# Performance work log

Measured on AMD Instinct MI355X. Metric: run time of the kernel, lower is better.

## Reference

```python
import jax, jax.numpy as jnp
import numpy as np

N, E, B = 16384, 65536, 32
D_IN, ED, H, L = 4, 5, 64, 3  # node feat, edge feat, hidden=output, num layers
NEG_SLOPE = 0.1
EPS = 1e-5


def _leaky(v):
    return jnp.where(v > 0, v, NEG_SLOPE * v)


def setup_inputs() -> dict:
    key = jax.random.key(0)
    ks = jax.random.split(key, 32)
    s = 0.05
    inp = {
        'x': jax.random.normal(ks[0], (N, D_IN), jnp.float32),
        'edge_index': jax.random.randint(ks[1], (2, E), 0, N),
        'edge_attr': jax.random.normal(ks[2], (E, ED), jnp.float32),
        'batch': jnp.sort(jax.random.randint(ks[3], (N,), 0, B)),
        # input projection Linear(4 -> H)
        'W_in': s * jax.random.normal(ks[4], (H, D_IN), jnp.float32),
        'b_in': jnp.zeros((H,), jnp.float32),
        # per-layer edge MLP: Linear(ED->H), Linear(H->H), Linear(H->H*H); stacked over L
        'ew1': s * jax.random.normal(ks[5], (L, H, ED), jnp.float32),
        'eb1': jnp.zeros((L, H), jnp.float32),
        'ew2': s * jax.random.normal(ks[6], (L, H, H), jnp.float32),
        'eb2': jnp.zeros((L, H), jnp.float32),
        'ew3': s * jax.random.normal(ks[7], (L, H * H, H), jnp.float32),
        'eb3': jnp.zeros((L, H * H), jnp.float32),
        # NNConv root weight + bias per layer
        'root_w': s * jax.random.normal(ks[8], (L, H, H), jnp.float32),
        'root_b': jnp.zeros((L, H), jnp.float32),
        # LayerNorm per layer
        'ln_g': jnp.ones((L, H), jnp.float32),
        'ln_b': jnp.zeros((L, H), jnp.float32),
        # prediction head: Linear(H->H), Linear(H->H//2), Linear(H//2->1)
        'pw1': s * jax.random.normal(ks[9], (H, H), jnp.float32),
        'pb1': jnp.zeros((H,), jnp.float32),
        'pw2': s * jax.random.normal(ks[10], (H // 2, H), jnp.float32),
        'pb2': jnp.zeros((H // 2,), jnp.float32),
        'pw3': s * jax.random.normal(ks[11], (1, H // 2), jnp.float32),
        'pb3': jnp.zeros((1,), jnp.float32),
    }
    return inp


def reference(x, edge_index, edge_attr, batch, W_in, b_in, ew1, eb1, ew2, eb2,
              ew3, eb3, root_w, root_b, ln_g, ln_b, pw1, pb1, pw2, pb2, pw3, pb3):
    src, dst = edge_index[0], edge_index[1]
    n_nodes = x.shape[0]
    n_edges = edge_attr.shape[0]
    # in-degree for scatter-mean (PyG yields 0 for isolated nodes)
    deg = jax.ops.segment_sum(jnp.ones((n_edges,), x.dtype), dst, num_segments=n_nodes)
    deg = jnp.maximum(deg, 1.0)[:, None]

    # input projection (dropout = identity in eval)
    h = _leaky(x @ W_in.T + b_in)

    for l in range(L):
        # edge MLP -> per-edge weight matrix [E, H, H]
        e = _leaky(edge_attr @ ew1[l].T + eb1[l])
        e = _leaky(e @ ew2[l].T + eb2[l])
        Wf = (e @ ew3[l].T + eb3[l]).reshape(n_edges, H, H)
        # message = x_src @ W_edge, scatter-mean to dst
        msg = jnp.einsum('ei,eio->eo', h[src], Wf)
        agg = jax.ops.segment_sum(msg, dst, num_segments=n_nodes) / deg
        out = agg + h @ root_w[l].T + root_b[l]
        # LayerNorm (post-norm)
        mu = out.mean(-1, keepdims=True)
        var = ((out - mu) ** 2).mean(-1, keepdims=True)
        out = (out - mu) * jax.lax.rsqrt(var + EPS) * ln_g[l] + ln_b[l]
        # activation + (identity) dropout + residual (in==out for all layers)
        h = _leaky(out) + h

    # global mean pool over graphs
    pooled = jax.ops.segment_sum(h, batch, num_segments=B)
    cnt = jax.ops.segment_sum(jnp.ones((n_nodes,), h.dtype), batch, num_segments=B)
    pooled = pooled / jnp.maximum(cnt, 1.0)[:, None]

    # prediction head
    p = _leaky(pooled @ pw1.T + pb1)
    p = _leaky(p @ pw2.T + pb2)
    pred = (p @ pw3.T + pb3).squeeze(-1)  # [B]
    return pred
```

## Files before the change

kernel.cpp:

```cpp
#include <hip/hip_runtime.h>
#include <hip/hip_bf16.h>

#define N_NODES 16384
#define N_EDGES 65536
#define NB      32
#define H       64
#define NLAYERS 3
#define NEG     0.1f
#define LN_EPS  1e-5f

typedef _Float16 f16;
typedef _Float16 f16x2 __attribute__((ext_vector_type(2)));
typedef _Float16 f16x8 __attribute__((ext_vector_type(8)));
typedef __fp16   hf16x2 __attribute__((ext_vector_type(2)));
typedef float    f32x16 __attribute__((ext_vector_type(16)));

union F16x8 { f16x8 v; f16x2 p[4]; int4 i4; int2 i2[2]; };
union F16x2U { f16x2 h2; hf16x2 raw; unsigned int u; };
union F16U   { f16 h; unsigned short u; };

__device__ __forceinline__ f16x2 pkrtz(float a, float b) {
    F16x2U t; t.raw = __builtin_amdgcn_cvt_pkrtz(a, b); return t.h2;
}
__device__ __forceinline__ float leaky(float v) { return v > 0.f ? v : NEG * v; }

__global__ __launch_bounds__(256) void k_setup(const float* __restrict__ x,
                                               const float* __restrict__ Win,
                                               const float* __restrict__ bin,
                                               const int* __restrict__ dst,
                                               const float* __restrict__ ew3,
                                               const float* __restrict__ eb3,
                                               float* __restrict__ h,
                                               float* __restrict__ deg,
                                               f16* __restrict__ Bp) {
    int bid = blockIdx.x;
    if (bid < 4096) {
        int t = bid * 256 + threadIdx.x;
        int n = t >> 6, j = t & 63;
        const float* xr = x + n * 4;
        const float* wr = Win + j * 4;
        float v = bin[j] + xr[0] * wr[0] + xr[1] * wr[1] + xr[2] * wr[2] + xr[3] * wr[3];
        h[t] = leaky(v);
    } else if (bid < 4352) {
        int e = (bid - 4096) * 256 + threadIdx.x;
        atomicAdd(&deg[dst[e]], 1.0f);
    } else {
        int tg    = (bid - 4352) * 256 + threadIdx.x;
        int lane  = tg & 63;
        int gslot = tg >> 6;
        int l     = gslot / 520;
        int slot  = gslot - l * 520;
        const float* ew3l = ew3 + (size_t)l * 262144;
        const float* eb3l = eb3 + (size_t)l * 4096;
        int i   = slot >> 3;
        int rem = slot & 7;
        int ks  = rem >> 1;
        int oq  = rem & 1;
        int o   = oq * 32 + (lane & 31);
        int k0  = ks * 16 + (lane >> 5) * 8;
        float v[8];
        if (i < 64) {
            const float* s = ew3l + ((size_t)(i * 64 + o)) * 64 + k0;
            float4 a = ((const float4*)s)[0];
            float4 b = ((const float4*)s)[1];
            v[0] = a.x; v[1] = a.y; v[2] = a.z; v[3] = a.w;
            v[4] = b.x; v[5] = b.y; v[6] = b.z; v[7] = b.w;
        } else {
#pragma unroll
            for (int j = 0; j < 8; j++) v[j] = eb3l[(k0 + j) * 64 + o];
        }
        union { int4 i4; f16 a[8]; } out;
#pragma unroll
        for (int j = 0; j < 8; j++) out.a[j] = (f16)v[j];
        *(int4*)(Bp + (size_t)l * 266240 + (size_t)slot * 512 + lane * 8) = out.i4;
    }
}

#define HS_STRIDE 76

__device__ __forceinline__ void loadB8(const f16* __restrict__ Bp, int c, int oq, int lane, F16x8* dstB) {
    const f16* base = Bp + (((size_t)(c * 16 + oq)) << 9) + lane * 8;
#pragma unroll
    for (int di = 0; di < 2; di++)
#pragma unroll
        for (int ks = 0; ks < 4; ks++)
            dstB[di * 4 + ks].i4 = *(const int4*)(base + ((di * 8 + ks * 2) << 9));
}
__device__ __forceinline__ void loadB4(const f16* __restrict__ Bp, int oq, int lane, F16x8* dstB) {
    const f16* base = Bp + (((size_t)(512 + oq)) << 9) + lane * 8;
#pragma unroll
    for (int ks = 0; ks < 4; ks++)
        dstB[ks].i4 = *(const int4*)(base + ((ks * 2) << 9));
}

__device__ __forceinline__ void msg_chunk2(int c, const F16x8* __restrict__ B,
                                           const unsigned short* hp0,
                                           const unsigned short* hp1,
                                           const f16x2 (*e2p)[4][4], f32x16* CC) {
    unsigned int rr0 = *(const unsigned int*)(hp0 + 2 * c);
    unsigned int rr1 = *(const unsigned int*)(hp1 + 2 * c);
    F16x2U h00, h01, h10, h11;
    h00.u = __builtin_amdgcn_perm(rr0, rr0, 0x01000100u);
    h10.u = __builtin_amdgcn_perm(rr0, rr0, 0x03020302u);
    h01.u = __builtin_amdgcn_perm(rr1, rr1, 0x01000100u);
    h11.u = __builtin_amdgcn_perm(rr1, rr1, 0x03020302u);
#pragma unroll
    for (int ks = 0; ks < 4; ks++) {
        F16x8 A00, A01, A10, A11;
#pragma unroll
        for (int r = 0; r < 4; r++) {
            A00.p[r] = h00.h2 * e2p[0][ks][r];
            A01.p[r] = h01.h2 * e2p[1][ks][r];
            A10.p[r] = h10.h2 * e2p[0][ks][r];
            A11.p[r] = h11.h2 * e2p[1][ks][r];
        }
        CC[0] = __builtin_amdgcn_mfma_f32_32x32x16_f16(A00.v, B[0 * 4 + ks].v, CC[0], 0, 0, 0);
        CC[1] = __builtin_amdgcn_mfma_f32_32x32x16_f16(A01.v, B[0 * 4 + ks].v, CC[1], 0, 0, 0);
        CC[2] = __builtin_amdgcn_mfma_f32_32x32x16_f16(A10.v, B[1 * 4 + ks].v, CC[2], 0, 0, 0);
        CC[3] = __builtin_amdgcn_mfma_f32_32x32x16_f16(A11.v, B[1 * 4 + ks].v, CC[3], 0, 0, 0);
    }
}

__global__ __launch_bounds__(256, 2) void k_msg(const float* __restrict__ h,
                                                const float* __restrict__ ea,
                                                const float* __restrict__ w1,
                                                const float* __restrict__ b1,
                                                const float* __restrict__ w2,
                                                const float* __restrict__ b2,
                                                const f16* __restrict__ Bp,
                                                const int* __restrict__ src,
                                                const int* __restrict__ dst,
                                                float* __restrict__ agg) {
    __shared__ __align__(16) unsigned short hsL[128 * HS_STRIDE];
    __shared__ __align__(16) unsigned short e1L[128 * 72];
    __shared__ __align__(16) unsigned short e2L[128 * 72];
    __shared__ float eas[128 * 8];
    __shared__ int dstL[128];

    const int t    = threadIdx.x;
    const int lane = t & 63;
    const int w    = t >> 6;
    const int eh   = w >> 1, oq = w & 1;
    const int m    = lane & 31;
    const int kp   = lane >> 5;
    const int eb   = blockIdx.x * 128;

    for (int idx = t; idx < 640; idx += 256) {
        int r = idx / 5, d = idx - r * 5;
        eas[r * 8 + d] = ea[(size_t)eb * 5 + idx];
    }
    {
        int e    = t >> 1;
        int half = t & 1;
        int nsrc = src[eb + e];
        const float4* hr = (const float4*)(h + (size_t)nsrc * 64 + half * 32);
        unsigned int* hrow = (unsigned int*)hsL + e * (HS_STRIDE / 2) + half * 16;
#pragma unroll
        for (int q = 0; q < 8; q++) {
            float4 v = hr[q];
            F16x2U p0, p1;
            p0.raw = __builtin_amdgcn_cvt_pkrtz(v.x, v.y);
            p1.raw = __builtin_amdgcn_cvt_pkrtz(v.z, v.w);
            hrow[q * 2 + 0] = p0.u;
            hrow[q * 2 + 1] = p1.u;
        }
        if (t < 128) dstL[t] = dst[eb + t];
    }
    __syncthreads();

    {
        int kk = t & 63;
        int eg = t >> 6;
        float w1r[5];
#pragma unroll
        for (int d = 0; d < 5; d++) w1r[d] = w1[kk * 5 + d];
        float b1r = b1[kk];
#pragma unroll 4
        for (int g = 0; g < 32; g++) {
            int row = eg * 32 + g;
            float4 a4 = *(const float4*)(eas + row * 8);
            float a5 = eas[row * 8 + 4];
            float v = b1r + a4.x * w1r[0] + a4.y * w1r[1] + a4.z * w1r[2] + a4.w * w1r[3] + a5 * w1r[4];
            F16U z; z.h = (f16)leaky(v);
            e1L[row * 72 + kk] = z.u;
        }
    }
    __syncthreads();

    {
        F16x8 W2f[4];
#pragma unroll
        for (int ks = 0; ks < 4; ks++) {
            const float* s = w2 + (size_t)(oq * 32 + m) * 64 + ks * 16 + kp * 8;
            float4 a = ((const float4*)s)[0];
            float4 b = ((const float4*)s)[1];
            W2f[ks].p[0] = pkrtz(a.x, a.y);
            W2f[ks].p[1] = pkrtz(a.z, a.w);
            W2f[ks].p[2] = pkrtz(b.x, b.y);
            W2f[ks].p[3] = pkrtz(b.z, b.w);
        }
        float b2r = b2[oq * 32 + m];
#pragma unroll
        for (int tt = 0; tt < 2; tt++) {
            f32x16 C2 = {0,0,0,0,0,0,0,0,0,0,0,0,0,0,0,0};
#pragma unroll
            for (int ks = 0; ks < 4; ks++) {
                F16x8 A;
                A.i4 = *(const int4*)(e1L + (size_t)((eh * 2 + tt) * 32 + m) * 72 + ks * 16 + kp * 8);
                C2 = __builtin_amdgcn_mfma_f32_32x32x16_f16(A.v, W2f[ks].v, C2, 0, 0, 0);
            }
#pragma unroll
            for (int reg = 0; reg < 16; reg++) {
                int r = (reg & 3) + 8 * (reg >> 2) + 4 * kp;
                F16U z; z.h = (f16)leaky(C2[reg] + b2r);
                e2L[((eh * 2 + tt) * 32 + r) * 72 + oq * 32 + m] = z.u;
            }
        }
    }
    __syncthreads();

    f16x2 e2p[2][4][4];
#pragma unroll
    for (int tt = 0; tt < 2; tt++) {
#pragma unroll
        for (int ks = 0; ks < 4; ks++) {
            F16x8 q;
            q.i4 = *(const int4*)(e2L + (size_t)((eh * 2 + tt) * 32 + m) * 72 + ks * 16 + kp * 8);
            e2p[tt][ks][0] = q.p[0]; e2p[tt][ks][1] = q.p[1];
            e2p[tt][ks][2] = q.p[2]; e2p[tt][ks][3] = q.p[3];
        }
    }

    f32x16 CC[4];
#pragma unroll
    for (int q = 0; q < 4; q++)
#pragma unroll
        for (int r = 0; r < 16; r++) CC[q][r] = 0.f;

    const unsigned short* hp0 = hsL + ((eh * 2 + 0) * 32 + m) * HS_STRIDE;
    const unsigned short* hp1 = hsL + ((eh * 2 + 1) * 32 + m) * HS_STRIDE;

    F16x8 B0[8], B1[8];
    loadB8(Bp, 0, oq, lane, B0);
    loadB8(Bp, 1, oq, lane, B1);
    for (int it = 0; it < 15; it++) {
        int c = it * 2;
        msg_chunk2(c,     B0, hp0, hp1, e2p, CC);  loadB8(Bp, c + 2, oq, lane, B0);
        msg_chunk2(c + 1, B1, hp0, hp1, e2p, CC);  loadB8(Bp, c + 3, oq, lane, B1);
    }
    msg_chunk2(30, B0, hp0, hp1, e2p, CC);
    loadB4(Bp, oq, lane, B0);
    msg_chunk2(31, B1, hp0, hp1, e2p, CC);

#pragma unroll
    for (int ks = 0; ks < 4; ks++) {
        int koff = (ks * 16 + kp * 8) * 2;
        const char* r0p = (const char*)hsL + (size_t)((eh * 2 + 0) * 32 + m) * (HS_STRIDE * 2) + koff;
        const char* r1p = (const char*)hsL + (size_t)((eh * 2 + 1) * 32 + m) * (HS_STRIDE * 2) + koff;
        F16x8 A0, A1;
        A0.i2[0] = *(const int2*)(r0p); A0.i2[1] = *(const int2*)(r0p + 8);
        A1.i2[0] = *(const int2*)(r1p); A1.i2[1] = *(const int2*)(r1p + 8);
        CC[0] = __builtin_amdgcn_mfma_f32_32x32x16_f16(A0.v, B0[ks].v, CC[0], 0, 0, 0);
        CC[1] = __builtin_amdgcn_mfma_f32_32x32x16_f16(A1.v, B0[ks].v, CC[1], 0, 0, 0);
    }

    int o = oq * 32 + m;
#pragma unroll
    for (int reg = 0; reg < 16; reg++) {
        int r = (reg & 3) + 8 * (reg >> 2) + 4 * kp;
        atomicAdd(&agg[(size_t)dstL[(eh * 2 + 0) * 32 + r] * 64 + o], CC[0][reg] + CC[2][reg]);
    }
#pragma unroll
    for (int reg = 0; reg < 16; reg++) {
        int r = (reg & 3) + 8 * (reg >> 2) + 4 * kp;
        atomicAdd(&agg[(size_t)dstL[(eh * 2 + 1) * 32 + r] * 64 + o], CC[1][reg] + CC[3][reg]);
    }
}

__global__ __launch_bounds__(512) void k_node(const float* __restrict__ agg,
                                              const float* __restrict__ deg,
                                              const float* __restrict__ rw,
                                              const float* __restrict__ rb,
                                              const float* __restrict__ lg,
                                              const float* __restrict__ lb,
                                              float* __restrict__ h,
                                              const int* __restrict__ batch,
                                              float* __restrict__ pooled,
                                              int last) {
    __shared__ __align__(16) unsigned short hA[64 * 72];
    __shared__ float outL[64][68];
    int t = threadIdx.x;
    int nb = blockIdx.x * 64;
    int lane = t & 63, w = t >> 6;
    int m = lane & 31, kp = lane >> 5;

    int node = t >> 3, c0 = (t & 7) * 8;
    size_t gb = (size_t)(nb + node) * 64 + c0;
    float4 ag0 = *(const float4*)(agg + gb);
    float4 ag1 = *(const float4*)(agg + gb + 4);
    float4 hp0 = *(const float4*)(h + gb);
    float4 hp1 = *(const float4*)(h + gb + 4);
    float  vdeg = fmaxf(deg[nb + node], 1.0f);
    float4 gv0 = *(const float4*)(lg + c0);
    float4 gv1 = *(const float4*)(lg + c0 + 4);
    float4 bv0 = *(const float4*)(lb + c0);
    float4 bv1 = *(const float4*)(lb + c0 + 4);

    {
        unsigned int* drow = (unsigned int*)hA + node * 36 + c0 / 2;
        F16x2U p0, p1, p2, p3;
        p0.raw = __builtin_amdgcn_cvt_pkrtz(hp0.x, hp0.y);
        p1.raw = __builtin_amdgcn_cvt_pkrtz(hp0.z, hp0.w);
        p2.raw = __builtin_amdgcn_cvt_pkrtz(hp1.x, hp1.y);
        p3.raw = __builtin_amdgcn_cvt_pkrtz(hp1.z, hp1.w);
        drow[0] = p0.u; drow[1] = p1.u; drow[2] = p2.u; drow[3] = p3.u;
    }
    F16x8 Bf[4];
    if (t < 256) {
        int oq = w & 1;
#pragma unroll
        for (int ks = 0; ks < 4; ks++) {
            const float* s = rw + (size_t)(oq * 32 + m) * 64 + ks * 16 + kp * 8;
            float4 a = ((const float4*)s)[0];
            float4 b = ((const float4*)s)[1];
            Bf[ks].p[0] = pkrtz(a.x, a.y);
            Bf[ks].p[1] = pkrtz(a.z, a.w);
            Bf[ks].p[2] = pkrtz(b.x, b.y);
            Bf[ks].p[3] = pkrtz(b.z, b.w);
        }
    }
    __syncthreads();

    if (t < 256) {
        int nq = w >> 1, oq = w & 1;
        f32x16 C = {0,0,0,0,0,0,0,0,0,0,0,0,0,0,0,0};
#pragma unroll
        for (int ks = 0; ks < 4; ks++) {
            F16x8 A;
            A.i4 = *(const int4*)(hA + (size_t)(nq * 32 + m) * 72 + ks * 16 + kp * 8);
            C = __builtin_amdgcn_mfma_f32_32x32x16_f16(A.v, Bf[ks].v, C, 0, 0, 0);
        }
        int o = oq * 32 + m;
        float rbv = rb[o];
#pragma unroll
        for (int reg = 0; reg < 16; reg++) {
            int r = (reg & 3) + 8 * (reg >> 2) + 4 * kp;
            outL[nq * 32 + r][o] = C[reg] + rbv;
        }
    }
    __syncthreads();

    {
        float v[8];
        v[0] = outL[node][c0 + 0] + ag0.x / vdeg;
        v[1] = outL[node][c0 + 1] + ag0.y / vdeg;
        v[2] = outL[node][c0 + 2] + ag0.z / vdeg;
        v[3] = outL[node][c0 + 3] + ag0.w / vdeg;
        v[4] = outL[node][c0 + 4] + ag1.x / vdeg;
        v[5] = outL[node][c0 + 5] + ag1.y / vdeg;
        v[6] = outL[node][c0 + 6] + ag1.z / vdeg;
        v[7] = outL[node][c0 + 7] + ag1.w / vdeg;
        float s = 0.f;
#pragma unroll
        for (int i = 0; i < 8; i++) s += v[i];
        s += __shfl_xor(s, 1);
        s += __shfl_xor(s, 2);
        s += __shfl_xor(s, 4);
        float mu = s * (1.f / 64.f);
        float vs = 0.f;
#pragma unroll
        for (int i = 0; i < 8; i++) { float d = v[i] - mu; vs += d * d; }
        vs += __shfl_xor(vs, 1);
        vs += __shfl_xor(vs, 2);
        vs += __shfl_xor(vs, 4);
        float rs = rsqrtf(vs * (1.f / 64.f) + LN_EPS);
        float gfv[8] = { gv0.x, gv0.y, gv0.z, gv0.w, gv1.x, gv1.y, gv1.z, gv1.w };
        float bfv[8] = { bv0.x, bv0.y, bv0.z, bv0.w, bv1.x, bv1.y, bv1.z, bv1.w };
        float hfv[8] = { hp0.x, hp0.y, hp0.z, hp0.w, hp1.x, hp1.y, hp1.z, hp1.w };
        float hn[8];
#pragma unroll
        for (int i = 0; i < 8; i++) {
            float ov = (v[i] - mu) * rs * gfv[i] + bfv[i];
            hn[i] = leaky(ov) + hfv[i];
        }
        float4 hw0, hw1;
        hw0.x = hn[0]; hw0.y = hn[1]; hw0.z = hn[2]; hw0.w = hn[3];
        hw1.x = hn[4]; hw1.y = hn[5]; hw1.z = hn[6]; hw1.w = hn[7];
        *(float4*)(h + gb)     = hw0;
        *(float4*)(h + gb + 4) = hw1;
#pragma unroll
        for (int i = 0; i < 8; i++) outL[node][c0 + i] = hn[i];
    }

    if (last) {
        __syncthreads();
        float accp = 0.f;
        int cur = batch[nb + w * 8];
        for (int q = 0; q < 8; q++) {
            int n = w * 8 + q;
            float hv = outL[n][lane];
            int b = batch[nb + n];
            if (b != cur) { atomicAdd(&pooled[cur * 64 + lane], accp); accp = 0.f; cur = b; }
            accp += hv;
        }
        atomicAdd(&pooled[cur * 64 + lane], accp);
    }
}

__global__ __launch_bounds__(256) void k_head(const float* __restrict__ pooled,
                                              const int* __restrict__ batch,
                                              const float* __restrict__ pw1, const float* __restrict__ pb1,
                                              const float* __restrict__ pw2, const float* __restrict__ pb2,
                                              const float* __restrict__ pw3, const float* __restrict__ pb3,
                                              float* __restrict__ out) {
    __shared__ float cntL[32];
    __shared__ float ps[32][64];
    __shared__ float p1[32][64];
    __shared__ float p2[32][32];
    int t = threadIdx.x;
    if (t < 32) cntL[t] = 0.f;
    __syncthreads();
    {
        const int4* bp4 = (const int4*)(batch + t * 64);
        int cur = batch[t * 64];
        float c = 0.f;
        for (int q = 0; q < 16; q++) {
            int4 b4 = bp4[q];
            int bs[4] = { b4.x, b4.y, b4.z, b4.w };
#pragma unroll
            for (int e = 0; e < 4; e++) {
                if (bs[e] != cur) { atomicAdd(&cntL[cur], c); cur = bs[e]; c = 0.f; }
                c += 1.f;
            }
        }
        atomicAdd(&cntL[cur], c);
    }
    __syncthreads();
    for (int idx = t; idx < 2048; idx += 256) {
        int b = idx >> 6, j = idx & 63;
        ps[b][j] = pooled[idx] / fmaxf(cntL[b], 1.0f);
    }
    __syncthreads();
    for (int idx = t; idx < 2048; idx += 256) {
        int b = idx >> 6, j = idx & 63;
        float v = pb1[j];
#pragma unroll 8
        for (int i = 0; i < 64; i++) v += ps[b][i] * pw1[j * 64 + i];
        p1[b][j] = leaky(v);
    }
    __syncthreads();
    for (int idx = t; idx < 1024; idx += 256) {
        int b = idx >> 5, j = idx & 31;
        float v = pb2[j];
#pragma unroll 8
        for (int i = 0; i < 64; i++) v += p1[b][i] * pw2[j * 64 + i];
        p2[b][j] = leaky(v);
    }
    __syncthreads();
    if (t < 32) {
        float v = pb3[0];
#pragma unroll 8
        for (int i = 0; i < 32; i++) v += p2[t][i] * pw3[i];
        out[t] = v;
    }
}

extern "C" void kernel_launch(void* const* d_in, const int* in_sizes, int n_in,
                              void* d_out, int out_size, void* d_ws, size_t ws_size,
                              hipStream_t stream) {
    const float* x    = (const float*)d_in[0];
    const int*   eidx = (const int*)  d_in[1];
    const float* ea   = (const float*)d_in[2];
    const int*   bat  = (const int*)  d_in[3];
    const float* Win  = (const float*)d_in[4];
    const float* bin  = (const float*)d_in[5];
    const float* ew1  = (const float*)d_in[6];
    const float* eb1  = (const float*)d_in[7];
    const float* ew2  = (const float*)d_in[8];
    const float* eb2  = (const float*)d_in[9];
    const float* ew3  = (const float*)d_in[10];
    const float* eb3  = (const float*)d_in[11];
    const float* rw   = (const float*)d_in[12];
    const float* rb   = (const float*)d_in[13];
    const float* lg   = (const float*)d_in[14];
    const float* lb   = (const float*)d_in[15];
    const float* pw1  = (const float*)d_in[16];
    const float* pb1  = (const float*)d_in[17];
    const float* pw2  = (const float*)d_in[18];
    const float* pb2  = (const float*)d_in[19];
    const float* pw3  = (const float*)d_in[20];
    const float* pb3  = (const float*)d_in[21];
    float* out = (float*)d_out;

    float* ws     = (float*)d_ws;
    float* h      = ws;
    float* agg    = ws + 1048576;
    float* deg    = ws + 4194304;
    float* pooled = ws + 4210688;
    f16*   Bp     = (f16*)(ws + 4212800);

    const int* srcp = eidx;
    const int* dstp = eidx + N_EDGES;

    (void)hipMemsetAsync(agg, 0, (size_t)3164224 * sizeof(float), stream);

    k_setup<<<4742, 256, 0, stream>>>(x, Win, bin, dstp, ew3, eb3, h, deg, Bp);

    for (int l = 0; l < NLAYERS; l++) {
        float* agg_l = agg + (size_t)l * N_NODES * H;
        k_msg <<<N_EDGES / 128, 256, 0, stream>>>(h, ea, ew1 + l * 320, eb1 + l * 64,
                                                  ew2 + l * 4096, eb2 + l * 64,
                                                  Bp + (size_t)l * 266240,
                                                  srcp, dstp, agg_l);
        k_node<<<N_NODES / 64, 512, 0, stream>>>(agg_l, deg, rw + l * 4096, rb + l * 64,
                                                 lg + l * 64, lb + l * 64, h,
                                                 bat, pooled, l == NLAYERS - 1 ? 1 : 0);
    }

    k_head<<<1, 256, 0, stream>>>(pooled, bat, pw1, pb1, pw2, pb2, pw3, pb3, out);
}
```

Baseline: 305.5 us.

## Fuse all GNN stages into one persistent cooperative kernel with grid syncs

Replaces the sequence of setup, per-layer message, per-layer node and head launches with a single cooperative kernel of 256 blocks × 512 threads. The phases are separated by grid-wide barriers, and shared memory is reused through a union. The message phase now handles 256 edges per block and stages the per-edge weight tiles into an LDS triple-buffer ring using global_load_lds, so loads overlap the MFMA work. The aim is to remove launch gaps and improve reuse of the B matrix. The costs are grid-sync overhead, lower occupancy from one large block per CU, and a fallback path to the old kernels if the cooperative launch fails.

```diff
diff --git a/kernel.cpp b/kernel.cpp
--- a/kernel.cpp
+++ b/kernel.cpp
@@ -1,5 +1,8 @@
 #include <hip/hip_runtime.h>
 #include <hip/hip_bf16.h>
+#include <hip/hip_cooperative_groups.h>
+
+namespace cg = cooperative_groups;
 
 #define N_NODES 16384
 #define N_EDGES 65536
@@ -23,6 +26,484 @@
     F16x2U t; t.raw = __builtin_amdgcn_cvt_pkrtz(a, b); return t.h2;
 }
 __device__ __forceinline__ float leaky(float v) { return v > 0.f ? v : NEG * v; }
+
+#define HS_STRIDE 76
+
+__device__ __forceinline__ void loadB8(const f16* __restrict__ Bp, int c, int oq, int lane, F16x8* dstB) {
+    const f16* base = Bp + (((size_t)(c * 16 + oq)) << 9) + lane * 8;
+#pragma unroll
+    for (int di = 0; di < 2; di++)
+#pragma unroll
+        for (int ks = 0; ks < 4; ks++)
+            dstB[di * 4 + ks].i4 = *(const int4*)(base + ((di * 8 + ks * 2) << 9));
+}
+__device__ __forceinline__ void loadB4(const f16* __restrict__ Bp, int oq, int lane, F16x8* dstB) {
+    const f16* base = Bp + (((size_t)(512 + oq)) << 9) + lane * 8;
+#pragma unroll
+    for (int ks = 0; ks < 4; ks++)
+        dstB[ks].i4 = *(const int4*)(base + ((ks * 2) << 9));
+}
+__device__ __forceinline__ void msg_chunk2(int c, const F16x8* __restrict__ B,
+                                           const unsigned short* hp0,
+                                           const unsigned short* hp1,
+                                           const f16x2 (*e2p)[4][4], f32x16* CC) {
+    unsigned int rr0 = *(const unsigned int*)(hp0 + 2 * c);
+    unsigned int rr1 = *(const unsigned int*)(hp1 + 2 * c);
+    F16x2U h00, h01, h10, h11;
+    h00.u = __builtin_amdgcn_perm(rr0, rr0, 0x01000100u);
+    h10.u = __builtin_amdgcn_perm(rr0, rr0, 0x03020302u);
+    h01.u = __builtin_amdgcn_perm(rr1, rr1, 0x01000100u);
+    h11.u = __builtin_amdgcn_perm(rr1, rr1, 0x03020302u);
+#pragma unroll
+    for (int ks = 0; ks < 4; ks++) {
+        F16x8 A00, A01, A10, A11;
+#pragma unroll
+        for (int r = 0; r < 4; r++) {
+            A00.p[r] = h00.h2 * e2p[0][ks][r];
+            A01.p[r] = h01.h2 * e2p[1][ks][r];
+            A10.p[r] = h10.h2 * e2p[0][ks][r];
+            A11.p[r] = h11.h2 * e2p[1][ks][r];
+        }
+        CC[0] = __builtin_amdgcn_mfma_f32_32x32x16_f16(A00.v, B[0 * 4 + ks].v, CC[0], 0, 0, 0);
+        CC[1] = __builtin_amdgcn_mfma_f32_32x32x16_f16(A01.v, B[0 * 4 + ks].v, CC[1], 0, 0, 0);
+        CC[2] = __builtin_amdgcn_mfma_f32_32x32x16_f16(A10.v, B[1 * 4 + ks].v, CC[2], 0, 0, 0);
+        CC[3] = __builtin_amdgcn_mfma_f32_32x32x16_f16(A11.v, B[1 * 4 + ks].v, CC[3], 0, 0, 0);
+    }
+}
+__device__ __forceinline__ void stageChunk(const f16* __restrict__ Bp, int c, f16* ring, int w, int lane) {
+    const f16* g = Bp + (((size_t)(c * 16 + w * 2)) << 9) + lane * 8;
+    f16* l = ring + (c % 3) * 8192 + ((w * 2) << 9);
+#pragma unroll
+    for (int s = 0; s < 2; s++)
+        __builtin_amdgcn_global_load_lds(
+            (const __attribute__((address_space(1))) unsigned int*)(g + (s << 9)),
+            (__attribute__((address_space(3))) unsigned int*)(l + (s << 9)), 16, 0, 0);
+}
+__device__ __forceinline__ void readBr(const f16* rslot, int oq, int lane, F16x8* Bf) {
+#pragma unroll
+    for (int di = 0; di < 2; di++)
+#pragma unroll
+        for (int ks = 0; ks < 4; ks++)
+            Bf[di * 4 + ks].i4 = *(const int4*)(rslot + ((di * 8 + ks * 2 + oq) << 9) + lane * 8);
+}
+
+struct MsgSh7 {
+    unsigned short hsL[256 * HS_STRIDE];
+    unsigned short eL[256 * 72];
+    f16 ring[3 * 8192];
+    int dstL[256];
+};
+struct NodeSh { unsigned short hA[64 * 72]; float outL[64][68]; };
+struct HeadSh { float cntL[32]; float ps[32][64]; float p1[32][64]; float p2[32][32]; };
+union ShU { MsgSh7 m; NodeSh n; HeadSh hd; };
+
+__device__ void msg_phase(MsgSh7& S,
+                          const float* __restrict__ h, const float* __restrict__ ea,
+                          const float* __restrict__ w1, const float* __restrict__ b1,
+                          const float* __restrict__ w2, const float* __restrict__ b2,
+                          const f16* __restrict__ Bp,
+                          const int* __restrict__ src, const int* __restrict__ dst,
+                          float* __restrict__ agg) {
+    const int t    = threadIdx.x;
+    const int lane = t & 63;
+    const int w    = t >> 6;
+    const int eh   = w >> 1, oq = w & 1;
+    const int m    = lane & 31;
+    const int kp   = lane >> 5;
+    const int eb   = blockIdx.x * 256;
+
+    stageChunk(Bp, 0, S.ring, w, lane);
+    stageChunk(Bp, 1, S.ring, w, lane);
+
+    {
+        int e    = t >> 1;
+        int half = t & 1;
+        int nsrc = src[eb + e];
+        const float4* hr = (const float4*)(h + (size_t)nsrc * 64 + half * 32);
+        unsigned int* hrow = (unsigned int*)S.hsL + e * (HS_STRIDE / 2) + half * 16;
+#pragma unroll
+        for (int q = 0; q < 8; q++) {
+            float4 v = hr[q];
+            F16x2U p0, p1;
+            p0.raw = __builtin_amdgcn_cvt_pkrtz(v.x, v.y);
+            p1.raw = __builtin_amdgcn_cvt_pkrtz(v.z, v.w);
+            hrow[q * 2 + 0] = p0.u;
+            hrow[q * 2 + 1] = p1.u;
+        }
+        if (t < 256) S.dstL[t] = dst[eb + t];
+    }
+
+    {
+        int kk = t & 63;
+        int eg = t >> 6;
+        float w1r[5];
+#pragma unroll
+        for (int d = 0; d < 5; d++) w1r[d] = w1[kk * 5 + d];
+        float b1r = b1[kk];
+        const float* ear = ea + (size_t)(eb + eg * 32) * 5;
+#pragma unroll 4
+        for (int g = 0; g < 32; g++) {
+            float a0 = ear[g * 5 + 0], a1 = ear[g * 5 + 1], a2 = ear[g * 5 + 2];
+            float a3 = ear[g * 5 + 3], a4 = ear[g * 5 + 4];
+            float v = b1r + a0 * w1r[0] + a1 * w1r[1] + a2 * w1r[2] + a3 * w1r[3] + a4 * w1r[4];
+            F16U z; z.h = (f16)leaky(v);
+            S.eL[(eg * 32 + g) * 72 + kk] = z.u;
+        }
+    }
+    __syncthreads();
+
+    {
+        F16x8 W2f[4];
+#pragma unroll
+        for (int ks = 0; ks < 4; ks++) {
+            const float* s = w2 + (size_t)(oq * 32 + m) * 64 + ks * 16 + kp * 8;
+            float4 a = ((const float4*)s)[0];
+            float4 b = ((const float4*)s)[1];
+            W2f[ks].p[0] = pkrtz(a.x, a.y);
+            W2f[ks].p[1] = pkrtz(a.z, a.w);
+            W2f[ks].p[2] = pkrtz(b.x, b.y);
+            W2f[ks].p[3] = pkrtz(b.z, b.w);
+        }
+        float b2r = b2[oq * 32 + m];
+        F16x8 A8[8];
+#pragma unroll
+        for (int tt = 0; tt < 2; tt++)
+#pragma unroll
+            for (int ks = 0; ks < 4; ks++)
+                A8[tt * 4 + ks].i4 = *(const int4*)(S.eL + (size_t)((eh * 2 + tt) * 32 + m) * 72 + ks * 16 + kp * 8);
+        __syncthreads();
+#pragma unroll
+        for (int tt = 0; tt < 2; tt++) {
+            f32x16 C2 = {0,0,0,0,0,0,0,0,0,0,0,0,0,0,0,0};
+#pragma unroll
+            for (int ks = 0; ks < 4; ks++)
+                C2 = __builtin_amdgcn_mfma_f32_32x32x16_f16(A8[tt * 4 + ks].v, W2f[ks].v, C2, 0, 0, 0);
+#pragma unroll
+            for (int reg = 0; reg < 16; reg++) {
+                int r = (reg & 3) + 8 * (reg >> 2) + 4 * kp;
+                F16U z; z.h = (f16)leaky(C2[reg] + b2r);
+                S.eL[((eh * 2 + tt) * 32 + r) * 72 + oq * 32 + m] = z.u;
+            }
+        }
+    }
+    __syncthreads();
+
+    f16x2 e2p[2][4][4];
+#pragma unroll
+    for (int tt = 0; tt < 2; tt++) {
+#pragma unroll
+        for (int ks = 0; ks < 4; ks++) {
+            F16x8 q;
+            q.i4 = *(const int4*)(S.eL + (size_t)((eh * 2 + tt) * 32 + m) * 72 + ks * 16 + kp * 8);
+            e2p[tt][ks][0] = q.p[0]; e2p[tt][ks][1] = q.p[1];
+            e2p[tt][ks][2] = q.p[2]; e2p[tt][ks][3] = q.p[3];
+        }
+    }
+
+    f32x16 CC[4];
+#pragma unroll
+    for (int q = 0; q < 4; q++)
+#pragma unroll
+        for (int r = 0; r < 16; r++) CC[q][r] = 0.f;
+
+    const unsigned short* hp0 = S.hsL + ((eh * 2 + 0) * 32 + m) * HS_STRIDE;
+    const unsigned short* hp1 = S.hsL + ((eh * 2 + 1) * 32 + m) * HS_STRIDE;
+
+    F16x8 Bf[8];
+#pragma unroll 1
+    for (int c = 0; c < 30; c++) {
+        asm volatile("s_waitcnt vmcnt(2)" ::: "memory");
+        __builtin_amdgcn_s_barrier();
+        stageChunk(Bp, c + 2, S.ring, w, lane);
+        readBr(S.ring + (c % 3) * 8192, oq, lane, Bf);
+        msg_chunk2(c, Bf, hp0, hp1, e2p, CC);
+    }
+    asm volatile("s_waitcnt vmcnt(2)" ::: "memory");
+    __builtin_amdgcn_s_barrier();
+    readBr(S.ring + (30 % 3) * 8192, oq, lane, Bf);
+    msg_chunk2(30, Bf, hp0, hp1, e2p, CC);
+    asm volatile("s_waitcnt vmcnt(0)" ::: "memory");
+    __builtin_amdgcn_s_barrier();
+    readBr(S.ring + (31 % 3) * 8192, oq, lane, Bf);
+    F16x8 Bb[4];
+    loadB4(Bp, oq, lane, Bb);
+    msg_chunk2(31, Bf, hp0, hp1, e2p, CC);
+
+#pragma unroll
+    for (int ks = 0; ks < 4; ks++) {
+        int koff = (ks * 16 + kp * 8) * 2;
+        const char* r0p = (const char*)S.hsL + (size_t)((eh * 2 + 0) * 32 + m) * (HS_STRIDE * 2) + koff;
+        const char* r1p = (const char*)S.hsL + (size_t)((eh * 2 + 1) * 32 + m) * (HS_STRIDE * 2) + koff;
+        F16x8 A0, A1;
+        A0.i2[0] = *(const int2*)(r0p); A0.i2[1] = *(const int2*)(r0p + 8);
+        A1.i2[0] = *(const int2*)(r1p); A1.i2[1] = *(const int2*)(r1p + 8);
+        CC[0] = __builtin_amdgcn_mfma_f32_32x32x16_f16(A0.v, Bb[ks].v, CC[0], 0, 0, 0);
+        CC[1] = __builtin_amdgcn_mfma_f32_32x32x16_f16(A1.v, Bb[ks].v, CC[1], 0, 0, 0);
+    }
+
+    int o = oq * 32 + m;
+#pragma unroll
+    for (int reg = 0; reg < 16; reg++) {
+        int r = (reg & 3) + 8 * (reg >> 2) + 4 * kp;
+        atomicAdd(&agg[(size_t)S.dstL[(eh * 2 + 0) * 32 + r] * 64 + o], CC[0][reg] + CC[2][reg]);
+    }
+#pragma unroll
+    for (int reg = 0; reg < 16; reg++) {
+        int r = (reg & 3) + 8 * (reg >> 2) + 4 * kp;
+        atomicAdd(&agg[(size_t)S.dstL[(eh * 2 + 1) * 32 + r] * 64 + o], CC[1][reg] + CC[3][reg]);
+    }
+}
+
+__device__ void node_phase(NodeSh& N,
+                           const float* __restrict__ agg, const float* __restrict__ deg,
+                           const float* __restrict__ rw, const float* __restrict__ rb,
+                           const float* __restrict__ lg, const float* __restrict__ lb,
+                           float* __restrict__ h, const int* __restrict__ batch,
+                           float* __restrict__ pooled, int last) {
+    int t = threadIdx.x;
+    int nb = blockIdx.x * 64;
+    int lane = t & 63, w = t >> 6;
+    int m = lane & 31, kp = lane >> 5;
+
+    int node = t >> 3, c0 = (t & 7) * 8;
+    size_t gb = (size_t)(nb + node) * 64 + c0;
+    float4 ag0 = *(const float4*)(agg + gb);
+    float4 ag1 = *(const float4*)(agg + gb + 4);
+    float4 hp0 = *(const float4*)(h + gb);
+    float4 hp1 = *(const float4*)(h + gb + 4);
+    float  vdeg = fmaxf(deg[nb + node], 1.0f);
+    float4 gv0 = *(const float4*)(lg + c0);
+    float4 gv1 = *(const float4*)(lg + c0 + 4);
+    float4 bv0 = *(const float4*)(lb + c0);
+    float4 bv1 = *(const float4*)(lb + c0 + 4);
+
+    {
+        unsigned int* drow = (unsigned int*)N.hA + node * 36 + c0 / 2;
+        F16x2U p0, p1, p2, p3;
+        p0.raw = __builtin_amdgcn_cvt_pkrtz(hp0.x, hp0.y);
+        p1.raw = __builtin_amdgcn_cvt_pkrtz(hp0.z, hp0.w);
+        p2.raw = __builtin_amdgcn_cvt_pkrtz(hp1.x, hp1.y);
+        p3.raw = __builtin_amdgcn_cvt_pkrtz(hp1.z, hp1.w);
+        drow[0] = p0.u; drow[1] = p1.u; drow[2] = p2.u; drow[3] = p3.u;
+    }
+    F16x8 Bf[4];
+    if (t < 256) {
+        int oq = w & 1;
+#pragma unroll
+        for (int ks = 0; ks < 4; ks++) {
+            const float* s = rw + (size_t)(oq * 32 + m) * 64 + ks * 16 + kp * 8;
+            float4 a = ((const float4*)s)[0];
+            float4 b = ((const float4*)s)[1];
+            Bf[ks].p[0] = pkrtz(a.x, a.y);
+            Bf[ks].p[1] = pkrtz(a.z, a.w);
+            Bf[ks].p[2] = pkrtz(b.x, b.y);
+            Bf[ks].p[3] = pkrtz(b.z, b.w);
+        }
+    }
+    __syncthreads();
+
+    if (t < 256) {
+        int nq = w >> 1, oq = w & 1;
+        f32x16 C = {0,0,0,0,0,0,0,0,0,0,0,0,0,0,0,0};
+#pragma unroll
+        for (int ks = 0; ks < 4; ks++) {
+            F16x8 A;
+            A.i4 = *(const int4*)(N.hA + (size_t)(nq * 32 + m) * 72 + ks * 16 + kp * 8);
+            C = __builtin_amdgcn_mfma_f32_32x32x16_f16(A.v, Bf[ks].v, C, 0, 0, 0);
+        }
+        int o = oq * 32 + m;
+        float rbv = rb[o];
+#pragma unroll
+        for (int reg = 0; reg < 16; reg++) {
+            int r = (reg & 3) + 8 * (reg >> 2) + 4 * kp;
+            N.outL[nq * 32 + r][o] = C[reg] + rbv;
+        }
+    }
+    __syncthreads();
+
+    {
+        float v[8];
+        v[0] = N.outL[node][c0 + 0] + ag0.x / vdeg;
+        v[1] = N.outL[node][c0 + 1] + ag0.y / vdeg;
+        v[2] = N.outL[node][c0 + 2] + ag0.z / vdeg;
+        v[3] = N.outL[node][c0 + 3] + ag0.w / vdeg;
+        v[4] = N.outL[node][c0 + 4] + ag1.x / vdeg;
+        v[5] = N.outL[node][c0 + 5] + ag1.y / vdeg;
+        v[6] = N.outL[node][c0 + 6] + ag1.z / vdeg;
+        v[7] = N.outL[node][c0 + 7] + ag1.w / vdeg;
+        float s = 0.f;
+#pragma unroll
+        for (int i = 0; i < 8; i++) s += v[i];
+        s += __shfl_xor(s, 1);
+        s += __shfl_xor(s, 2);
+        s += __shfl_xor(s, 4);
+        float mu = s * (1.f / 64.f);
+        float vs = 0.f;
+#pragma unroll
+        for (int i = 0; i < 8; i++) { float d = v[i] - mu; vs += d * d; }
+        vs += __shfl_xor(vs, 1);
+        vs += __shfl_xor(vs, 2);
+        vs += __shfl_xor(vs, 4);
+        float rs = rsqrtf(vs * (1.f / 64.f) + LN_EPS);
+        float gfv[8] = { gv0.x, gv0.y, gv0.z, gv0.w, gv1.x, gv1.y, gv1.z, gv1.w };
+        float bfv[8] = { bv0.x, bv0.y, bv0.z, bv0.w, bv1.x, bv1.y, bv1.z, bv1.w };
+        float hfv[8] = { hp0.x, hp0.y, hp0.z, hp0.w, hp1.x, hp1.y, hp1.z, hp1.w };
+        float hn[8];
+#pragma unroll
+        for (int i = 0; i < 8; i++) {
+            float ov = (v[i] - mu) * rs * gfv[i] + bfv[i];
+            hn[i] = leaky(ov) + hfv[i];
+        }
+        float4 hw0, hw1;
+        hw0.x = hn[0]; hw0.y = hn[1]; hw0.z = hn[2]; hw0.w = hn[3];
+        hw1.x = hn[4]; hw1.y = hn[5]; hw1.z = hn[6]; hw1.w = hn[7];
+        *(float4*)(h + gb)     = hw0;
+        *(float4*)(h + gb + 4) = hw1;
+#pragma unroll
+        for (int i = 0; i < 8; i++) N.outL[node][c0 + i] = hn[i];
+    }
+
+    if (last) {
+        __syncthreads();
+        float accp = 0.f;
+        int cur = batch[nb + w * 8];
+        for (int q = 0; q < 8; q++) {
+            int n = w * 8 + q;
+            float hv = N.outL[n][lane];
+            int b = batch[nb + n];
+            if (b != cur) { atomicAdd(&pooled[cur * 64 + lane], accp); accp = 0.f; cur = b; }
+            accp += hv;
+        }
+        atomicAdd(&pooled[cur * 64 + lane], accp);
+    }
+}
+
+__global__ __launch_bounds__(512) void k_fused(
+    const float* __restrict__ x, const float* __restrict__ ea,
+    const int* __restrict__ src, const int* __restrict__ dst, const int* __restrict__ bat,
+    const float* __restrict__ Win, const float* __restrict__ bin,
+    const float* __restrict__ ew1, const float* __restrict__ eb1,
+    const float* __restrict__ ew2, const float* __restrict__ eb2,
+    const float* __restrict__ ew3, const float* __restrict__ eb3,
+    const float* __restrict__ rw, const float* __restrict__ rb,
+    const float* __restrict__ lg, const float* __restrict__ lb,
+    const float* __restrict__ pw1, const float* __restrict__ pb1,
+    const float* __restrict__ pw2, const float* __restrict__ pb2,
+    const float* __restrict__ pw3, const float* __restrict__ pb3,
+    float* __restrict__ h, float* __restrict__ agg, float* __restrict__ deg,
+    float* __restrict__ pooled, f16* __restrict__ Bp, float* __restrict__ out) {
+
+    __shared__ __align__(16) ShU sh;
+    cg::grid_group grid = cg::this_grid();
+
+    const int t    = threadIdx.x;
+    const int lane = t & 63;
+    const int w    = t >> 6;
+
+    {
+        int tg = blockIdx.x * 512 + t;
+#pragma unroll
+        for (int r = 0; r < 8; r++) {
+            int idx = r * 131072 + tg;
+            int n = idx >> 6, j = idx & 63;
+            const float* xr = x + n * 4;
+            const float* wr = Win + j * 4;
+            float v = bin[j] + xr[0] * wr[0] + xr[1] * wr[1] + xr[2] * wr[2] + xr[3] * wr[3];
+            h[idx] = leaky(v);
+        }
+        if (tg < N_EDGES) atomicAdd(&deg[dst[tg]], 1.0f);
+        int wid = blockIdx.x * 8 + w;
+        if (wid < 1560) {
+            int l    = wid / 520;
+            int slot = wid - l * 520;
+            const float* ew3l = ew3 + (size_t)l * 262144;
+            const float* eb3l = eb3 + (size_t)l * 4096;
+            int i   = slot >> 3;
+            int rem = slot & 7;
+            int ks  = rem >> 1;
+            int oq  = rem & 1;
+            int o   = oq * 32 + (lane & 31);
+            int k0  = ks * 16 + (lane >> 5) * 8;
+            float v[8];
+            if (i < 64) {
+                const float* s = ew3l + ((size_t)(i * 64 + o)) * 64 + k0;
+                float4 a = ((const float4*)s)[0];
+                float4 b = ((const float4*)s)[1];
+                v[0] = a.x; v[1] = a.y; v[2] = a.z; v[3] = a.w;
+                v[4] = b.x; v[5] = b.y; v[6] = b.z; v[7] = b.w;
+            } else {
+#pragma unroll
+                for (int j = 0; j < 8; j++) v[j] = eb3l[(k0 + j) * 64 + o];
+            }
+            union { int4 i4; f16 a[8]; } ov;
+#pragma unroll
+            for (int j = 0; j < 8; j++) ov.a[j] = (f16)v[j];
+            *(int4*)(Bp + (size_t)l * 266240 + (size_t)slot * 512 + lane * 8) = ov.i4;
+        }
+    }
+    grid.sync();
+
+    for (int l = 0; l < NLAYERS; l++) {
+        float* agg_l = agg + (size_t)l * N_NODES * H;
+        msg_phase(sh.m, h, ea, ew1 + l * 320, eb1 + l * 64,
+                  ew2 + l * 4096, eb2 + l * 64,
+                  Bp + (size_t)l * 266240, src, dst, agg_l);
+        grid.sync();
+        node_phase(sh.n, agg_l, deg, rw + l * 4096, rb + l * 64,
+                   lg + l * 64, lb + l * 64, h, bat, pooled,
+                   l == NLAYERS - 1 ? 1 : 0);
+        grid.sync();
+    }
+
+    if (blockIdx.x == 0) {
+        HeadSh& Hh = sh.hd;
+        if (t < 32) Hh.cntL[t] = 0.f;
+        __syncthreads();
+        {
+            const int4* bp4 = (const int4*)(bat + t * 32);
+            int cur = bat[t * 32];
+            float c = 0.f;
+            for (int q = 0; q < 8; q++) {
+                int4 b4 = bp4[q];
+                int bs[4] = { b4.x, b4.y, b4.z, b4.w };
+#pragma unroll
+                for (int e = 0; e < 4; e++) {
+                    if (bs[e] != cur) { atomicAdd(&Hh.cntL[cur], c); cur = bs[e]; c = 0.f; }
+                    c += 1.f;
+                }
+            }
+            atomicAdd(&Hh.cntL[cur], c);
+        }
+        __syncthreads();
+        for (int idx = t; idx < 2048; idx += 512) {
+            int b = idx >> 6, j = idx & 63;
+            Hh.ps[b][j] = pooled[idx] / fmaxf(Hh.cntL[b], 1.0f);
+        }
+        __syncthreads();
+        for (int idx = t; idx < 2048; idx += 512) {
+            int b = idx >> 6, j = idx & 63;
+            float v = pb1[j];
+#pragma unroll 8
+            for (int i = 0; i < 64; i++) v += Hh.ps[b][i] * pw1[j * 64 + i];
+            Hh.p1[b][j] = leaky(v);
+        }
+        __syncthreads();
+        for (int idx = t; idx < 1024; idx += 512) {
+            int b = idx >> 5, j = idx & 31;
+            float v = pb2[j];
+#pragma unroll 8
+            for (int i = 0; i < 64; i++) v += Hh.p1[b][i] * pw2[j * 64 + i];
+            Hh.p2[b][j] = leaky(v);
+        }
+        __syncthreads();
+        if (t < 32) {
+            float v = pb3[0];
+#pragma unroll 8
+            for (int i = 0; i < 32; i++) v += Hh.p2[t][i] * pw3[i];
+            out[t] = v;
+        }
+    }
+}
 
 __global__ __launch_bounds__(256) void k_setup(const float* __restrict__ x,
                                                const float* __restrict__ Win,
@@ -69,55 +550,10 @@
 #pragma unroll
             for (int j = 0; j < 8; j++) v[j] = eb3l[(k0 + j) * 64 + o];
         }
-        union { int4 i4; f16 a[8]; } out;
-#pragma unroll
-        for (int j = 0; j < 8; j++) out.a[j] = (f16)v[j];
-        *(int4*)(Bp + (size_t)l * 266240 + (size_t)slot * 512 + lane * 8) = out.i4;
-    }
-}
-
-#define HS_STRIDE 76
-
-__device__ __forceinline__ void loadB8(const f16* __restrict__ Bp, int c, int oq, int lane, F16x8* dstB) {
-    const f16* base = Bp + (((size_t)(c * 16 + oq)) << 9) + lane * 8;
-#pragma unroll
-    for (int di = 0; di < 2; di++)
-#pragma unroll
-        for (int ks = 0; ks < 4; ks++)
-            dstB[di * 4 + ks].i4 = *(const int4*)(base + ((di * 8 + ks * 2) << 9));
-}
-__device__ __forceinline__ void loadB4(const f16* __restrict__ Bp, int oq, int lane, F16x8* dstB) {
-    const f16* base = Bp + (((size_t)(512 + oq)) << 9) + lane * 8;
-#pragma unroll
-    for (int ks = 0; ks < 4; ks++)
-        dstB[ks].i4 = *(const int4*)(base + ((ks * 2) << 9));
-}
-
-__device__ __forceinline__ void msg_chunk2(int c, const F16x8* __restrict__ B,
-                                           const unsigned short* hp0,
-                                           const unsigned short* hp1,
-                                           const f16x2 (*e2p)[4][4], f32x16* CC) {
-    unsigned int rr0 = *(const unsigned int*)(hp0 + 2 * c);
-    unsigned int rr1 = *(const unsigned int*)(hp1 + 2 * c);
-    F16x2U h00, h01, h10, h11;
-    h00.u = __builtin_amdgcn_perm(rr0, rr0, 0x01000100u);
-    h10.u = __builtin_amdgcn_perm(rr0, rr0, 0x03020302u);
-    h01.u = __builtin_amdgcn_perm(rr1, rr1, 0x01000100u);
-    h11.u = __builtin_amdgcn_perm(rr1, rr1, 0x03020302u);
-#pragma unroll
-    for (int ks = 0; ks < 4; ks++) {
-        F16x8 A00, A01, A10, A11;
-#pragma unroll
-        for (int r = 0; r < 4; r++) {
-            A00.p[r] = h00.h2 * e2p[0][ks][r];
-            A01.p[r] = h01.h2 * e2p[1][ks][r];
-            A10.p[r] = h10.h2 * e2p[0][ks][r];
-            A11.p[r] = h11.h2 * e2p[1][ks][r];
-        }
-        CC[0] = __builtin_amdgcn_mfma_f32_32x32x16_f16(A00.v, B[0 * 4 + ks].v, CC[0], 0, 0, 0);
-        CC[1] = __builtin_amdgcn_mfma_f32_32x32x16_f16(A01.v, B[0 * 4 + ks].v, CC[1], 0, 0, 0);
-        CC[2] = __builtin_amdgcn_mfma_f32_32x32x16_f16(A10.v, B[1 * 4 + ks].v, CC[2], 0, 0, 0);
-        CC[3] = __builtin_amdgcn_mfma_f32_32x32x16_f16(A11.v, B[1 * 4 + ks].v, CC[3], 0, 0, 0);
+        union { int4 i4; f16 a[8]; } outv;
+#pragma unroll
+        for (int j = 0; j < 8; j++) outv.a[j] = (f16)v[j];
+        *(int4*)(Bp + (size_t)l * 266240 + (size_t)slot * 512 + lane * 8) = outv.i4;
     }
 }
 
@@ -287,124 +723,8 @@
                                               const int* __restrict__ batch,
                                               float* __restrict__ pooled,
                                               int last) {
-    __shared__ __align__(16) unsigned short hA[64 * 72];
-    __shared__ float outL[64][68];
-    int t = threadIdx.x;
-    int nb = blockIdx.x * 64;
-    int lane = t & 63, w = t >> 6;
-    int m = lane & 31, kp = lane >> 5;
-
-    int node = t >> 3, c0 = (t & 7) * 8;
-    size_t gb = (size_t)(nb + node) * 64 + c0;
-    float4 ag0 = *(const float4*)(agg + gb);
-    float4 ag1 = *(const float4*)(agg + gb + 4);
-    float4 hp0 = *(const float4*)(h + gb);
-    float4 hp1 = *(const float4*)(h + gb + 4);
-    float  vdeg = fmaxf(deg[nb + node], 1.0f);
-    float4 gv0 = *(const float4*)(lg + c0);
-    float4 gv1 = *(const float4*)(lg + c0 + 4);
-    float4 bv0 = *(const float4*)(lb + c0);
-    float4 bv1 = *(const float4*)(lb + c0 + 4);
-
-    {
-        unsigned int* drow = (unsigned int*)hA + node * 36 + c0 / 2;
-        F16x2U p0, p1, p2, p3;
-        p0.raw = __builtin_amdgcn_cvt_pkrtz(hp0.x, hp0.y);
-        p1.raw = __builtin_amdgcn_cvt_pkrtz(hp0.z, hp0.w);
-        p2.raw = __builtin_amdgcn_cvt_pkrtz(hp1.x, hp1.y);
-        p3.raw = __builtin_amdgcn_cvt_pkrtz(hp1.z, hp1.w);
-        drow[0] = p0.u; drow[1] = p1.u; drow[2] = p2.u; drow[3] = p3.u;
-    }
-    F16x8 Bf[4];
-    if (t < 256) {
-        int oq = w & 1;
-#pragma unroll
-        for (int ks = 0; ks < 4; ks++) {
-            const float* s = rw + (size_t)(oq * 32 + m) * 64 + ks * 16 + kp * 8;
-            float4 a = ((const float4*)s)[0];
-            float4 b = ((const float4*)s)[1];
-            Bf[ks].p[0] = pkrtz(a.x, a.y);
-            Bf[ks].p[1] = pkrtz(a.z, a.w);
-            Bf[ks].p[2] = pkrtz(b.x, b.y);
-            Bf[ks].p[3] = pkrtz(b.z, b.w);
-        }
-    }
-    __syncthreads();
-
-    if (t < 256) {
-        int nq = w >> 1, oq = w & 1;
-        f32x16 C = {0,0,0,0,0,0,0,0,0,0,0,0,0,0,0,0};
-#pragma unroll
-        for (int ks = 0; ks < 4; ks++) {
-            F16x8 A;
-            A.i4 = *(const int4*)(hA + (size_t)(nq * 32 + m) * 72 + ks * 16 + kp * 8);
-            C = __builtin_amdgcn_mfma_f32_32x32x16_f16(A.v, Bf[ks].v, C, 0, 0, 0);
-        }
-        int o = oq * 32 + m;
-        float rbv = rb[o];
-#pragma unroll
-        for (int reg = 0; reg < 16; reg++) {
-            int r = (reg & 3) + 8 * (reg >> 2) + 4 * kp;
-            outL[nq * 32 + r][o] = C[reg] + rbv;
-        }
-    }
-    __syncthreads();
-
-    {
-        float v[8];
-        v[0] = outL[node][c0 + 0] + ag0.x / vdeg;
-        v[1] = outL[node][c0 + 1] + ag0.y / vdeg;
-        v[2] = outL[node][c0 + 2] + ag0.z / vdeg;
-        v[3] = outL[node][c0 + 3] + ag0.w / vdeg;
-        v[4] = outL[node][c0 + 4] + ag1.x / vdeg;
-        v[5] = outL[node][c0 + 5] + ag1.y / vdeg;
-        v[6] = outL[node][c0 + 6] + ag1.z / vdeg;
-        v[7] = outL[node][c0 + 7] + ag1.w / vdeg;
-        float s = 0.f;
-#pragma unroll
-        for (int i = 0; i < 8; i++) s += v[i];
-        s += __shfl_xor(s, 1);
-        s += __shfl_xor(s, 2);
-        s += __shfl_xor(s, 4);
-        float mu = s * (1.f / 64.f);
-        float vs = 0.f;
-#pragma unroll
-        for (int i = 0; i < 8; i++) { float d = v[i] - mu; vs += d * d; }
-        vs += __shfl_xor(vs, 1);
-        vs += __shfl_xor(vs, 2);
-        vs += __shfl_xor(vs, 4);
-        float rs = rsqrtf(vs * (1.f / 64.f) + LN_EPS);
-        float gfv[8] = { gv0.x, gv0.y, gv0.z, gv0.w, gv1.x, gv1.y, gv1.z, gv1.w };
-        float bfv[8] = { bv0.x, bv0.y, bv0.z, bv0.w, bv1.x, bv1.y, bv1.z, bv1.w };
-        float hfv[8] = { hp0.x, hp0.y, hp0.z, hp0.w, hp1.x, hp1.y, hp1.z, hp1.w };
-        float hn[8];
-#pragma unroll
-        for (int i = 0; i < 8; i++) {
-            float ov = (v[i] - mu) * rs * gfv[i] + bfv[i];
-            hn[i] = leaky(ov) + hfv[i];
-        }
-        float4 hw0, hw1;
-        hw0.x = hn[0]; hw0.y = hn[1]; hw0.z = hn[2]; hw0.w = hn[3];
-        hw1.x = hn[4]; hw1.y = hn[5]; hw1.z = hn[6]; hw1.w = hn[7];
-        *(float4*)(h + gb)     = hw0;
-        *(float4*)(h + gb + 4) = hw1;
-#pragma unroll
-        for (int i = 0; i < 8; i++) outL[node][c0 + i] = hn[i];
-    }
-
-    if (last) {
-        __syncthreads();
-        float accp = 0.f;
-        int cur = batch[nb + w * 8];
-        for (int q = 0; q < 8; q++) {
-            int n = w * 8 + q;
-            float hv = outL[n][lane];
-            int b = batch[nb + n];
-            if (b != cur) { atomicAdd(&pooled[cur * 64 + lane], accp); accp = 0.f; cur = b; }
-            accp += hv;
-        }
-        atomicAdd(&pooled[cur * 64 + lane], accp);
-    }
+    __shared__ __align__(16) NodeSh N;
+    node_phase(N, agg, deg, rw, rb, lg, lb, h, batch, pooled, last);
 }
 
 __global__ __launch_bounds__(256) void k_head(const float* __restrict__ pooled,
@@ -504,18 +824,30 @@
 
     (void)hipMemsetAsync(agg, 0, (size_t)3164224 * sizeof(float), stream);
 
-    k_setup<<<4742, 256, 0, stream>>>(x, Win, bin, dstp, ew3, eb3, h, deg, Bp);
-
-    for (int l = 0; l < NLAYERS; l++) {
-        float* agg_l = agg + (size_t)l * N_NODES * H;
-        k_msg <<<N_EDGES / 128, 256, 0, stream>>>(h, ea, ew1 + l * 320, eb1 + l * 64,
-                                                  ew2 + l * 4096, eb2 + l * 64,
-                                                  Bp + (size_t)l * 266240,
-                                                  srcp, dstp, agg_l);
-        k_node<<<N_NODES / 64, 512, 0, stream>>>(agg_l, deg, rw + l * 4096, rb + l * 64,
-                                                 lg + l * 64, lb + l * 64, h,
-                                                 bat, pooled, l == NLAYERS - 1 ? 1 : 0);
-    }
-
-    k_head<<<1, 256, 0, stream>>>(pooled, bat, pw1, pb1, pw2, pb2, pw3, pb3, out);
-}
+    void* args[] = {
+        (void*)&x, (void*)&ea, (void*)&srcp, (void*)&dstp, (void*)&bat,
+        (void*)&Win, (void*)&bin,
+        (void*)&ew1, (void*)&eb1, (void*)&ew2, (void*)&eb2,
+        (void*)&ew3, (void*)&eb3,
+        (void*)&rw, (void*)&rb, (void*)&lg, (void*)&lb,
+        (void*)&pw1, (void*)&pb1, (void*)&pw2, (void*)&pb2,
+        (void*)&pw3, (void*)&pb3,
+        (void*)&h, (void*)&agg, (void*)&deg, (void*)&pooled, (void*)&Bp, (void*)&out
+    };
+    hipError_t err = hipLaunchCooperativeKernel((void*)k_fused, dim3(256), dim3(512),
+                                                args, 0, stream);
+    if (err != hipSuccess) {
+        k_setup<<<4742, 256, 0, stream>>>(x, Win, bin, dstp, ew3, eb3, h, deg, Bp);
+        for (int l = 0; l < NLAYERS; l++) {
+            float* agg_l = agg + (size_t)l * N_NODES * H;
+            k_msg <<<N_EDGES / 128, 256, 0, stream>>>(h, ea, ew1 + l * 320, eb1 + l * 64,
+                                                      ew2 + l * 4096, eb2 + l * 64,
+                                                      Bp + (size_t)l * 266240,
+                                                      srcp, dstp, agg_l);
+            k_node<<<N_NODES / 64, 512, 0, stream>>>(agg_l, deg, rw + l * 4096, rb + l * 64,
+                                                     lg + l * 64, lb + l * 64, h,
+                                                     bat, pooled, l == NLAYERS - 1 ? 1 : 0);
+        }
+        k_head<<<1, 256, 0, stream>>>(pooled, bat, pw1, pb1, pw2, pb2, pw3, pb3, out);
+    }
+}
```

Measured after the change: 525.7 us. 72.1% more time.
